# Kernel optimization log

Measured on AMD Instinct MI355X. Metric: run time of the kernel, lower is better.

Reference implementation:

```python
import jax, jax.numpy as jnp
import numpy as np

B, NQ, NK, C = 16, 8, 4096, 256
H = W = 64
HEADS = 8
CI = 128          # embedding_dim // attention_downsample_rate
HD = CI // HEADS  # per-head dim
EPS = float(np.finfo(np.float32).tiny)


def _gumbel_topk(scores, noise, n):
    # iterative gumbel-softmax top-k relaxation with straight-through hard k-hot
    g = scores + noise
    khot = jnp.zeros_like(g)
    onehot = jnp.zeros_like(g)
    for _ in range(n):
        g = g + jnp.log(jnp.maximum(1.0 - onehot, EPS))
        onehot = jax.nn.softmax(g, axis=-1)
        khot = khot + onehot
    _, ind = jax.lax.top_k(khot, n)
    rows = jnp.arange(khot.shape[0])[:, None]
    hard = jnp.zeros_like(khot).at[rows, ind].set(1.0)
    ret = hard - jax.lax.stop_gradient(khot) + khot  # == hard numerically
    return ret, jnp.sort(ind, axis=1)  # sorted idx = row-major order of boolean-mask select


def _sample_points(pe, content, ret, idx):
    # pe [H,W,C], content [b,H,W,C], ret [b,HW] k-hot, idx [b,k] sorted
    b = ret.shape[0]
    m = ret.reshape(b, H, W, 1)
    pe_m = (pe[None] * m).reshape(b, H * W, -1)
    c_m = (content * m).reshape(b, H * W, -1)
    take = lambda a: jnp.take_along_axis(a, idx[:, :, None], axis=1)
    return take(pe_m), take(c_m)


def _mlp(x, W1, b1, W2, b2, W3, b3):
    x = jax.nn.relu(x @ W1 + b1)
    x = jax.nn.relu(x @ W2 + b2)
    return x @ W3 + b3


def _forward(queries, keys, query_pe, key_pe, guiding_embedding, gumbel_p, gumbel_n,
             static_uncertain, static_refined, Wq, bq, Wk, bk, Wv, bv, Wo, bo,
             uW1, ub1, uW2, ub2, uW3, ub3, rW1, rb1, rW2, rb2, rW3, rb3,
             pe_gauss, point_pos, point_neg, n_sample_points):
    b = queries.shape[0]
    g = guiding_embedding.reshape(b, C, H * W).transpose(0, 2, 1)  # [b, HW, C]
    g = g * keys  # elementwise gating -> new guiding embedding

    # cross attention token -> image (internal dim CI, HEADS heads)
    def split_heads(x, Wx, bx):
        return (x @ Wx + bx).reshape(b, -1, HEADS, HD).transpose(0, 2, 1, 3)
    qh = split_heads(queries + query_pe, Wq, bq)
    kh = split_heads(g + key_pe, Wk, bk)
    vh = split_heads(g, Wv, bv)
    attn = jax.nn.softmax(jnp.einsum('bhqd,bhkd->bhqk', qh, kh) / np.float32(np.sqrt(HD)), axis=-1)
    out = jnp.einsum('bhqk,bhkd->bhqd', attn, vh).transpose(0, 2, 1, 3).reshape(b, -1, CI)
    queries = out @ Wo + bo  # [b, NQ, C]

    q1 = queries[:, 1, :]
    unc_tok = _mlp(jnp.concatenate([jnp.broadcast_to(static_uncertain, (b, C)), q1], -1),
                   uW1, ub1, uW2, ub2, uW3, ub3)
    ref_tok = _mlp(jnp.concatenate([jnp.broadcast_to(static_refined, (b, C)), q1], -1),
                   rW1, rb1, rW2, rb2, rW3, rb3)

    img = g.transpose(0, 2, 1)  # [b, C, HW]
    unc_norm = jax.nn.sigmoid(jnp.einsum('bc,bcn->bn', unc_tok, img))
    ref_mask = jnp.einsum('bc,bcn->bn', ref_tok, img)
    coarse_mask = jnp.einsum('bc,bcn->bn', q1, img)

    queries = jnp.concatenate([queries[:, 0:1], ref_tok[:, None, :], queries[:, 2:]], axis=1)

    # point-sampling reference map + gumbel-softmax top-k (training-path math)
    ref_map = unc_norm * (jax.nn.sigmoid(ref_mask) - jax.nn.sigmoid(coarse_mask))  # [b, HW]
    ret_p, idx_p = _gumbel_topk(ref_map, gumbel_p, n_sample_points)
    ret_n, idx_n = _gumbel_topk(-ref_map, gumbel_n, n_sample_points)

    # random fourier positional encoding of the 64x64 grid (SAM PositionEmbeddingRandom)
    xs = (jnp.arange(W, dtype=jnp.float32) + 0.5) / W
    ys = (jnp.arange(H, dtype=jnp.float32) + 0.5) / H
    coords = jnp.stack([jnp.tile(xs[None, :], (H, 1)), jnp.tile(ys[:, None], (1, W))], axis=-1)
    proj = ((2.0 * coords - 1.0) @ pe_gauss) * np.float32(2.0 * np.pi)  # [H, W, C//2]
    pe = jnp.concatenate([jnp.sin(proj), jnp.cos(proj)], axis=-1)       # [H, W, C]

    # F.interpolate of a 64x64 map to (64,64) is the identity here
    content = (keys + g).reshape(b, H, W, C)

    sp_pe, sp_c = _sample_points(pe, content, ret_p, idx_p)
    sn_pe, sn_c = _sample_points(pe, content, ret_n, idx_n)
    sp_pe = sp_pe + point_pos  # prompt_encoder.point_embeddings[1]
    sn_pe = sn_pe + point_neg  # prompt_encoder.point_embeddings[0]

    query_pe = jnp.concatenate([query_pe, sp_pe, sn_pe], axis=1)
    queries = jnp.concatenate([queries, sp_c, sn_c], axis=1)
    # pack (queries, query_pe) into one array for a single-output reference
    return jnp.concatenate([queries, query_pe], axis=1)  # [b, 2*(NQ+2k), C]


def setup_inputs():
    key = jax.random.key(0)
    ks = iter(jax.random.split(key, 48))
    n = lambda shape, s=1.0: jax.random.normal(next(ks), shape, jnp.float32) * s
    z = lambda shape: jnp.zeros(shape, jnp.float32)
    return {
        'queries': n((B, NQ, C)),
        'keys': n((B, NK, C)),
        'query_pe': n((B, NQ, C)),
        'key_pe': n((B, NK, C)),
        'guiding_embedding': n((B, C, H, W)),
        'gumbel_p': jax.random.gumbel(next(ks), (B, NK), jnp.float32),
        'gumbel_n': jax.random.gumbel(next(ks), (B, NK), jnp.float32),
        'static_uncertain': n((C,), 0.02),
        'static_refined': n((C,), 0.02),
        'Wq': n((C, CI), 0.02), 'bq': z((CI,)),
        'Wk': n((C, CI), 0.02), 'bk': z((CI,)),
        'Wv': n((C, CI), 0.02), 'bv': z((CI,)),
        'Wo': n((CI, C), 0.02), 'bo': z((C,)),
        'uW1': n((2 * C, C // 4), 0.05), 'ub1': z((C // 4,)),
        'uW2': n((C // 4, C // 4), 0.05), 'ub2': z((C // 4,)),
        'uW3': n((C // 4, C), 0.05), 'ub3': z((C,)),
        'rW1': n((2 * C, C // 4), 0.05), 'rb1': z((C // 4,)),
        'rW2': n((C // 4, C // 4), 0.05), 'rb2': z((C // 4,)),
        'rW3': n((C // 4, C), 0.05), 'rb3': z((C,)),
        'pe_gauss': n((2, C // 2)),
        'point_pos': n((C,), 0.02),
        'point_neg': n((C,), 0.02),
        'n_sample_points': 4,
    }


def reference(queries, keys, query_pe, key_pe, guiding_embedding, gumbel_p, gumbel_n,
              static_uncertain, static_refined, Wq, bq, Wk, bk, Wv, bv, Wo, bo,
              uW1, ub1, uW2, ub2, uW3, ub3, rW1, rb1, rW2, rb2, rW3, rb3,
              pe_gauss, point_pos, point_neg, n_sample_points):
    return _forward(queries, keys, query_pe, key_pe, guiding_embedding, gumbel_p, gumbel_n,
                    static_uncertain, static_refined, Wq, bq, Wk, bk, Wv, bv, Wo, bo,
                    uW1, ub1, uW2, ub2, uW3, ub3, rW1, rb1, rW2, rb2, rW3, rb3,
                    pe_gauss, point_pos, point_neg, n_sample_points)
```

## Files before the change

kernel.cpp:

```cpp
#include <hip/hip_runtime.h>

#define BB 16
#define NQn 8
#define NK 4096
#define CC 256
#define NHEADS 8
#define CIn 128
#define HDn 16
#define NHQ 64
#define EPS_TINY 1.17549435e-38f

constexpr size_t OFF_QK   = 0;
constexpr size_t OFF_QBK  = OFF_QK  + (size_t)BB*CC*NHQ;
constexpr size_t OFF_SC   = OFF_QBK + (size_t)BB*NHQ;
constexpr size_t OFF_MP   = OFF_SC  + (size_t)BB*NK*NHQ;
constexpr size_t OFF_SP   = OFF_MP  + (size_t)BB*32*NHQ;
constexpr size_t OFF_M    = OFF_SP  + (size_t)BB*32*NHQ;
constexpr size_t OFF_RS   = OFF_M   + (size_t)BB*NHQ;
constexpr size_t OFF_AVP  = OFF_RS  + (size_t)BB*NHQ;
constexpr size_t OFF_QATT = OFF_AVP + (size_t)BB*16*NHQ*CC;
constexpr size_t OFF_UNC  = OFF_QATT+ (size_t)BB*NQn*CC;
constexpr size_t OFF_REFT = OFF_UNC + (size_t)BB*CC;
constexpr size_t OFF_RMAP = OFF_REFT+ (size_t)BB*CC;
constexpr size_t OFF_IDX  = OFF_RMAP+ (size_t)BB*NK;
constexpr size_t OFF_RV   = OFF_IDX + 128;
constexpr size_t OFF_G    = OFF_RV  + 128;

__global__ __launch_bounds__(256) void k1_qside(
    const float* __restrict__ queries, const float* __restrict__ query_pe,
    const float* __restrict__ Wq, const float* __restrict__ bq,
    const float* __restrict__ Wk, const float* __restrict__ bk,
    float* __restrict__ ws)
{
  int b = blockIdx.x >> 3, q = blockIdx.x & 7, t = threadIdx.x;
  __shared__ float x[CC];
  __shared__ float qh[CIn];
  x[t] = queries[(b*NQn+q)*CC + t] + query_pe[(b*NQn+q)*CC + t];
  __syncthreads();
  if (t < CIn) {
    float a = bq[t];
    for (int c = 0; c < CC; ++c) a += x[c]*Wq[c*CIn + t];
    qh[t] = a * 0.25f;
  }
  __syncthreads();
  float* Qk = ws + OFF_QK;
  #pragma unroll
  for (int h = 0; h < NHEADS; ++h) {
    float a = 0.f;
    #pragma unroll
    for (int d = 0; d < HDn; ++d) a += qh[h*HDn+d] * Wk[t*CIn + h*HDn + d];
    Qk[((size_t)b*CC + t)*NHQ + h*NQn + q] = a;
  }
  if (t < NHEADS) {
    float a = 0.f;
    #pragma unroll
    for (int d = 0; d < HDn; ++d) a += qh[t*HDn+d] * bk[t*HDn+d];
    (ws + OFF_QBK)[b*NHQ + t*NQn + q] = a;
  }
}

__global__ __launch_bounds__(256) void k2_scores(
    const float* __restrict__ keys, const float* __restrict__ key_pe,
    const float* __restrict__ guiding, float* __restrict__ ws)
{
  int b = blockIdx.y, n0 = blockIdx.x * 64, t = threadIdx.x;
  __shared__ __align__(16) float Xs[64][36];
  __shared__ __align__(16) float Qs[32][64];
  __shared__ float Gt[32][65];
  const float* Qk = ws + OFF_QK + (size_t)b*CC*NHQ;
  float* G = ws + OFF_G;
  int tx = t & 15, ty = t >> 4;
  int xr  = t >> 3;
  int xc4 = (t & 7) * 4;
  int lane = t & 63, wv = t >> 6;
  float acc[4][4] = {};

  for (int c0 = 0; c0 < CC; c0 += 32) {
    size_t base0 = ((size_t)b*NK + n0 + xr)*CC + c0 + xc4;
    size_t base1 = base0 + (size_t)32*CC;
    float4 kp0 = *(const float4*)&keys[base0];
    float4 kp1 = *(const float4*)&keys[base1];
    float4 pp0 = *(const float4*)&key_pe[base0];
    float4 pp1 = *(const float4*)&key_pe[base1];
    float qp[8];
    #pragma unroll
    for (int i = 0; i < 8; ++i) {
      int l = i*256 + t;
      qp[i] = Qk[(size_t)(c0 + (l>>6))*NHQ + (l & 63)];
    }
    #pragma unroll
    for (int i = 0; i < 8; ++i)
      Gt[wv*8 + i][lane] = guiding[((size_t)b*CC + c0 + wv*8 + i)*NK + n0 + lane];
    __syncthreads();
    #pragma unroll
    for (int i = 0; i < 8; ++i) {
      int l = i*256 + t;
      Qs[l>>6][l&63] = qp[i];
    }
    {
      float4 g0, g1;
      g0.x = kp0.x * Gt[xc4+0][xr];    g0.y = kp0.y * Gt[xc4+1][xr];
      g0.z = kp0.z * Gt[xc4+2][xr];    g0.w = kp0.w * Gt[xc4+3][xr];
      g1.x = kp1.x * Gt[xc4+0][xr+32]; g1.y = kp1.y * Gt[xc4+1][xr+32];
      g1.z = kp1.z * Gt[xc4+2][xr+32]; g1.w = kp1.w * Gt[xc4+3][xr+32];
      *(float4*)&G[base0] = g0;
      *(float4*)&G[base1] = g1;
      float4 x0, x1;
      x0.x = g0.x+pp0.x; x0.y = g0.y+pp0.y; x0.z = g0.z+pp0.z; x0.w = g0.w+pp0.w;
      x1.x = g1.x+pp1.x; x1.y = g1.y+pp1.y; x1.z = g1.z+pp1.z; x1.w = g1.w+pp1.w;
      *(float4*)&Xs[xr][xc4]    = x0;
      *(float4*)&Xs[xr+32][xc4] = x1;
    }
    __syncthreads();
    #pragma unroll
    for (int cb = 0; cb < 8; ++cb) {
      float4 xf[4];
      #pragma unroll
      for (int i = 0; i < 4; ++i) xf[i] = *(const float4*)&Xs[4*ty+i][4*cb];
      #pragma unroll
      for (int u = 0; u < 4; ++u) {
        float4 qf = *(const float4*)&Qs[4*cb+u][4*tx];
        float xu[4] = { ((const float*)&xf[0])[u], ((const float*)&xf[1])[u],
                        ((const float*)&xf[2])[u], ((const float*)&xf[3])[u] };
        float qu[4] = { qf.x, qf.y, qf.z, qf.w };
        #pragma unroll
        for (int i = 0; i < 4; ++i)
          #pragma unroll
          for (int j = 0; j < 4; ++j) acc[i][j] += xu[i]*qu[j];
      }
    }
  }
  const float* qbk = ws + OFF_QBK + (size_t)b*NHQ;
  float qb[4] = {qbk[4*tx], qbk[4*tx+1], qbk[4*tx+2], qbk[4*tx+3]};
  float* sc = ws + OFF_SC + ((size_t)b*NK + n0)*NHQ;
  #pragma unroll
  for (int i = 0; i < 4; ++i) {
    float4 o;
    o.x = acc[i][0]+qb[0]; o.y = acc[i][1]+qb[1]; o.z = acc[i][2]+qb[2]; o.w = acc[i][3]+qb[3];
    *(float4*)&sc[(4*ty + i)*NHQ + 4*tx] = o;
  }
}

__global__ __launch_bounds__(256) void k3a_stats(float* __restrict__ ws)
{
  int b = blockIdx.y, sb = blockIdx.x, t = threadIdx.x;
  int hq = t & 63, r = t >> 6;
  const float* sc = ws + OFF_SC + ((size_t)b*NK + sb*128)*NHQ;
  float m = -INFINITY, s = 0.f;
  for (int i = 0; i < 32; ++i) {
    float v = sc[(r + 4*i)*NHQ + hq];
    if (v > m) { s = s*expf(m - v) + 1.f; m = v; } else { s += expf(v - m); }
  }
  __shared__ float rm[256], rs[256];
  rm[t] = m; rs[t] = s;
  __syncthreads();
  if (t < 64) {
    float m0=rm[t], m1=rm[t+64], m2=rm[t+128], m3=rm[t+192];
    float mm = fmaxf(fmaxf(m0,m1), fmaxf(m2,m3));
    float ss = rs[t]*expf(m0-mm) + rs[t+64]*expf(m1-mm) + rs[t+128]*expf(m2-mm) + rs[t+192]*expf(m3-mm);
    (ws + OFF_MP)[(b*32 + sb)*NHQ + t] = mm;
    (ws + OFF_SP)[(b*32 + sb)*NHQ + t] = ss;
  }
}

__global__ __launch_bounds__(64) void k3b_combine(float* __restrict__ ws)
{
  int b = blockIdx.x, hq = threadIdx.x;
  const float* mp = ws + OFF_MP + (size_t)b*32*NHQ;
  const float* sp = ws + OFF_SP + (size_t)b*32*NHQ;
  float m = -INFINITY;
  #pragma unroll
  for (int i = 0; i < 32; ++i) m = fmaxf(m, mp[i*NHQ+hq]);
  float s = 0.f;
  #pragma unroll
  for (int i = 0; i < 32; ++i) s += sp[i*NHQ+hq]*expf(mp[i*NHQ+hq]-m);
  (ws+OFF_M)[b*NHQ+hq] = m;
  (ws+OFF_RS)[b*NHQ+hq] = 1.0f/s;
}

__global__ __launch_bounds__(256) void k4_av(float* __restrict__ ws)
{
  int kb = blockIdx.x, ch = blockIdx.y, b = blockIdx.z, t = threadIdx.x;
  int k0 = kb * 256, cbase = ch * 64;
  __shared__ __align__(16) float gld[32][68];
  __shared__ __align__(16) float wld[32][64];
  __shared__ float mv[64], rv[64];
  if (t < 64) { mv[t] = (ws+OFF_M)[b*NHQ+t]; rv[t] = (ws+OFF_RS)[b*NHQ+t]; }
  int hq0 = (t & 15) * 4, c0 = (t >> 4) * 4;
  int sr = t >> 4, sc4 = (t & 15) * 4;
  float accf[4][4] = {};
  const float* sc = ws + OFF_SC;
  const float* G  = ws + OFF_G;
  __syncthreads();
  for (int kk = 0; kk < 256; kk += 32) {
    #pragma unroll
    for (int p = 0; p < 2; ++p)
      *(float4*)&gld[p*16 + sr][sc4] =
        *(const float4*)&G[((size_t)b*NK + k0+kk + p*16 + sr)*CC + cbase + sc4];
    #pragma unroll
    for (int i = 0; i < 8; ++i) {
      int l = i*256 + t; int k = l >> 6, hq = l & 63;
      float v = sc[((size_t)b*NK + k0+kk+k)*NHQ + hq];
      wld[k][hq] = expf(v - mv[hq]) * rv[hq];
    }
    __syncthreads();
    #pragma unroll 4
    for (int k = 0; k < 32; ++k) {
      float4 w4 = *(const float4*)&wld[k][hq0];
      float4 gv = *(const float4*)&gld[k][c0];
      float wq[4] = {w4.x, w4.y, w4.z, w4.w};
      float gq[4] = {gv.x, gv.y, gv.z, gv.w};
      #pragma unroll
      for (int i = 0; i < 4; ++i)
        #pragma unroll
        for (int j = 0; j < 4; ++j) accf[i][j] += wq[i]*gq[j];
    }
    __syncthreads();
  }
  float* avp = ws + OFF_AVP + (((size_t)b*16 + kb)*NHQ)*CC;
  #pragma unroll
  for (int i = 0; i < 4; ++i) {
    float4 o;
    o.x = accf[i][0]; o.y = accf[i][1]; o.z = accf[i][2]; o.w = accf[i][3];
    *(float4*)&avp[(size_t)(hq0 + i)*CC + cbase + c0] = o;
  }
}

__global__ __launch_bounds__(256) void k56_attout(
    const float* __restrict__ Wv, const float* __restrict__ bv,
    const float* __restrict__ Wo, const float* __restrict__ bo,
    float* __restrict__ ws)
{
  int b = blockIdx.x >> 3, q = blockIdx.x & 7, t = threadIdx.x;
  __shared__ float avs[NHEADS][CC];
  __shared__ float outv[CIn];
  const float* avp = ws + OFF_AVP;
  #pragma unroll
  for (int h = 0; h < NHEADS; ++h) {
    int hq = h*NQn + q;
    float a = 0.f;
    #pragma unroll 4
    for (int kb = 0; kb < 16; ++kb)
      a += avp[(((size_t)b*16 + kb)*NHQ + hq)*CC + t];
    avs[h][t] = a;
  }
  __syncthreads();
  if (t < CIn) {
    int h = t >> 4;
    float a = bv[t];
    for (int c = 0; c < CC; ++c) a += avs[h][c]*Wv[c*CIn + t];
    outv[t] = a;
  }
  __syncthreads();
  float a = bo[t];
  for (int ci = 0; ci < CIn; ++ci) a += outv[ci]*Wo[ci*CC + t];
  (ws+OFF_QATT)[((size_t)b*NQn + q)*CC + t] = a;
}

__global__ __launch_bounds__(256) void k7_mlps(
    const float* __restrict__ su, const float* __restrict__ sr,
    const float* __restrict__ uW1, const float* __restrict__ ub1,
    const float* __restrict__ uW2, const float* __restrict__ ub2,
    const float* __restrict__ uW3, const float* __restrict__ ub3,
    const float* __restrict__ rW1, const float* __restrict__ rb1,
    const float* __restrict__ rW2, const float* __restrict__ rb2,
    const float* __restrict__ rW3, const float* __restrict__ rb3,
    float* __restrict__ ws)
{
  int b = blockIdx.x, t = threadIdx.x;
  __shared__ float xs[768];
  __shared__ float h1[2][64], h2[2][64];
  xs[t] = su[t];
  xs[256+t] = (ws+OFF_QATT)[((size_t)b*NQn + 1)*CC + t];
  xs[512+t] = sr[t];
  __syncthreads();
  if (t < 128) {
    int which = t >> 6, o = t & 63;
    const float* W1 = which ? rW1 : uW1;
    const float* b1 = which ? rb1 : ub1;
    int base = which ? 512 : 0;
    float a = b1[o];
    for (int i = 0; i < 256; ++i) a += xs[base+i]*W1[i*64 + o];
    for (int i = 0; i < 256; ++i) a += xs[256+i]*W1[(256+i)*64 + o];
    h1[which][o] = fmaxf(a, 0.f);
  }
  __syncthreads();
  if (t < 128) {
    int which = t >> 6, o = t & 63;
    const float* W2 = which ? rW2 : uW2;
    const float* b2 = which ? rb2 : ub2;
    float a = b2[o];
    #pragma unroll 8
    for (int i = 0; i < 64; ++i) a += h1[which][i]*W2[i*64+o];
    h2[which][o] = fmaxf(a, 0.f);
  }
  __syncthreads();
  {
    float a = ub3[t];
    #pragma unroll 8
    for (int i = 0; i < 64; ++i) a += h2[0][i]*uW3[i*CC + t];
    (ws+OFF_UNC)[b*CC + t] = a;
    float a2 = rb3[t];
    #pragma unroll 8
    for (int i = 0; i < 64; ++i) a2 += h2[1][i]*rW3[i*CC + t];
    (ws+OFF_REFT)[b*CC + t] = a2;
  }
}

__global__ __launch_bounds__(256) void k8_masks(float* __restrict__ ws)
{
  int b = blockIdx.y, t = threadIdx.x;
  int wave = t >> 6, lane = t & 63;
  __shared__ float q1s[CC], us[CC], rts[CC];
  q1s[t] = (ws+OFF_QATT)[((size_t)b*NQn+1)*CC + t];
  us[t]  = (ws+OFF_UNC)[b*CC + t];
  rts[t] = (ws+OFF_REFT)[b*CC + t];
  __syncthreads();
  float q1v[4], usv[4], rtv[4];
  #pragma unroll
  for (int u = 0; u < 4; ++u) {
    q1v[u] = q1s[lane*4+u]; usv[u] = us[lane*4+u]; rtv[u] = rts[lane*4+u];
  }
  const float* G = ws + OFF_G;
  float* rmap = ws + OFF_RMAP + (size_t)b*NK;
  int n_base = blockIdx.x*64 + wave*16;
  for (int r = 0; r < 16; ++r) {
    int n = n_base + r;
    float4 gv = *(const float4*)&G[((size_t)b*NK + n)*CC + lane*4];
    float aq = gv.x*q1v[0] + gv.y*q1v[1] + gv.z*q1v[2] + gv.w*q1v[3];
    float au = gv.x*usv[0] + gv.y*usv[1] + gv.z*usv[2] + gv.w*usv[3];
    float ar = gv.x*rtv[0] + gv.y*rtv[1] + gv.z*rtv[2] + gv.w*rtv[3];
    #pragma unroll
    for (int s = 1; s < 64; s <<= 1) {
      aq += __shfl_xor(aq, s, 64);
      au += __shfl_xor(au, s, 64);
      ar += __shfl_xor(ar, s, 64);
    }
    if (lane == 0) {
      float un = 1.f/(1.f+expf(-au));
      rmap[n] = un * (1.f/(1.f+expf(-ar)) - 1.f/(1.f+expf(-aq)));
    }
  }
}

__global__ __launch_bounds__(256) void k9_gumbel(
    const float* __restrict__ gp, const float* __restrict__ gn,
    float* __restrict__ ws)
{
  int sign = blockIdx.x, b = blockIdx.y, t = threadIdx.x;
  int wave = t >> 6, lane = t & 63;
  const float* noise = sign ? gn : gp;
  const float* rmap = ws + OFF_RMAP + (size_t)b*NK;
  float g[16], kh[16], oh[16];
  #pragma unroll
  for (int i = 0; i < 16; ++i) {
    int n = i*256 + t;
    float scv = rmap[n];
    if (sign) scv = -scv;
    g[i] = scv + noise[(size_t)b*NK + n];
    kh[i] = 0.f; oh[i] = 0.f;
  }
  __shared__ float wred[8];
  __shared__ float selV[16];
  __shared__ int   selIdx[16];
  for (int it = 0; it < 4; ++it) {
    if (it > 0) {
      #pragma unroll
      for (int i = 0; i < 16; ++i) g[i] += logf(fmaxf(1.f - oh[i], EPS_TINY));
    }
    float m = g[0];
    #pragma unroll
    for (int i = 1; i < 16; ++i) m = fmaxf(m, g[i]);
    #pragma unroll
    for (int s = 1; s < 64; s <<= 1) m = fmaxf(m, __shfl_xor(m, s, 64));
    if (lane == 0) wred[wave] = m;
    __syncthreads();
    m = fmaxf(fmaxf(wred[0], wred[1]), fmaxf(wred[2], wred[3]));
    float e[16], ls = 0.f;
    #pragma unroll
    for (int i = 0; i < 16; ++i) { e[i] = expf(g[i]-m); ls += e[i]; }
    #pragma unroll
    for (int s = 1; s < 64; s <<= 1) ls += __shfl_xor(ls, s, 64);
    if (lane == 0) wred[4+wave] = ls;
    __syncthreads();
    float ssum = wred[4]+wred[5]+wred[6]+wred[7];
    #pragma unroll
    for (int i = 0; i < 16; ++i) { oh[i] = e[i]/ssum; kh[i] += oh[i]; }
  }
  int id[4]; float rr[4];
  for (int j = 0; j < 4; ++j) {
    float bv = kh[0]; int bi = t;
    #pragma unroll
    for (int i = 1; i < 16; ++i) {
      if (kh[i] > bv) { bv = kh[i]; bi = i*256 + t; }
    }
    #pragma unroll
    for (int s = 1; s < 64; s <<= 1) {
      float ov = __shfl_xor(bv, s, 64);
      int   oi = __shfl_xor(bi, s, 64);
      if (ov > bv || (ov == bv && oi < bi)) { bv = ov; bi = oi; }
    }
    if (lane == 0) { selV[j*4+wave] = bv; selIdx[j*4+wave] = bi; }
    __syncthreads();
    bv = selV[j*4]; bi = selIdx[j*4];
    #pragma unroll
    for (int w = 1; w < 4; ++w) {
      float ov = selV[j*4+w]; int oi = selIdx[j*4+w];
      if (ov > bv || (ov == bv && oi < bi)) { bv = ov; bi = oi; }
    }
    id[j] = bi; rr[j] = (1.f - bv) + bv;
    if ((bi & 255) == t) kh[bi >> 8] = -1.f;
  }
  if (t == 0) {
    for (int a = 0; a < 3; ++a)
      for (int c2 = a+1; c2 < 4; ++c2)
        if (id[c2] < id[a]) { int ti=id[a]; id[a]=id[c2]; id[c2]=ti; float tr=rr[a]; rr[a]=rr[c2]; rr[c2]=tr; }
    int* iout = (int*)(ws + OFF_IDX);
    float* rout = ws + OFF_RV;
    for (int j = 0; j < 4; ++j) {
      iout[(sign*BB + b)*4 + j] = id[j];
      rout[(sign*BB + b)*4 + j] = rr[j];
    }
  }
}

__global__ __launch_bounds__(256) void k10_out(
    const float* __restrict__ keys, const float* __restrict__ query_pe,
    const float* __restrict__ point_pos, const float* __restrict__ point_neg,
    const float* __restrict__ pe_gauss,
    float* __restrict__ ws, float* __restrict__ out)
{
  int b = blockIdx.y, r = blockIdx.x, t = threadIdx.x;
  const float* G = ws + OFF_G;
  float val;
  if (r < 8) {
    val = (r == 1) ? (ws+OFF_REFT)[b*CC + t]
                   : (ws+OFF_QATT)[((size_t)b*NQn + r)*CC + t];
  } else if (r < 16) {
    int j = r - 8; int sign = j >> 2; int jj = j & 3;
    int idx = ((const int*)(ws+OFF_IDX))[(sign*BB + b)*4 + jj];
    float rvv = (ws+OFF_RV)[(sign*BB + b)*4 + jj];
    float kv = keys[((size_t)b*NK + idx)*CC + t];
    float gv = G[((size_t)b*NK + idx)*CC + t];
    val = (kv + gv) * rvv;
  } else if (r < 24) {
    val = query_pe[((size_t)b*NQn + (r-16))*CC + t];
  } else {
    int j = r - 24; int sign = j >> 2; int jj = j & 3;
    int idx = ((const int*)(ws+OFF_IDX))[(sign*BB + b)*4 + jj];
    float rvv = (ws+OFF_RV)[(sign*BB + b)*4 + jj];
    const float* point = sign ? point_neg : point_pos;
    int h = idx >> 6, w = idx & 63;
    float x = (w + 0.5f)/64.f, y = (h + 0.5f)/64.f;
    int jf = (t < 128) ? t : (t - 128);
    float proj = ((2.f*x - 1.f)*pe_gauss[jf] + (2.f*y - 1.f)*pe_gauss[128 + jf]) * 6.28318530717958647692f;
    float sv = (t < 128) ? sinf(proj) : cosf(proj);
    val = sv*rvv + point[t];
  }
  out[((size_t)b*32 + r)*CC + t] = val;
}

extern "C" void kernel_launch(void* const* d_in, const int* in_sizes, int n_in,
                              void* d_out, int out_size, void* d_ws, size_t ws_size,
                              hipStream_t stream)
{
  const float* queries   = (const float*)d_in[0];
  const float* keys      = (const float*)d_in[1];
  const float* query_pe  = (const float*)d_in[2];
  const float* key_pe    = (const float*)d_in[3];
  const float* guiding   = (const float*)d_in[4];
  const float* gumbel_p  = (const float*)d_in[5];
  const float* gumbel_n  = (const float*)d_in[6];
  const float* s_unc     = (const float*)d_in[7];
  const float* s_ref     = (const float*)d_in[8];
  const float* Wq  = (const float*)d_in[9];   const float* bq  = (const float*)d_in[10];
  const float* Wk  = (const float*)d_in[11];  const float* bk  = (const float*)d_in[12];
  const float* Wv  = (const float*)d_in[13];  const float* bv  = (const float*)d_in[14];
  const float* Wo  = (const float*)d_in[15];  const float* bo  = (const float*)d_in[16];
  const float* uW1 = (const float*)d_in[17];  const float* ub1 = (const float*)d_in[18];
  const float* uW2 = (const float*)d_in[19];  const float* ub2 = (const float*)d_in[20];
  const float* uW3 = (const float*)d_in[21];  const float* ub3 = (const float*)d_in[22];
  const float* rW1 = (const float*)d_in[23];  const float* rb1 = (const float*)d_in[24];
  const float* rW2 = (const float*)d_in[25];  const float* rb2 = (const float*)d_in[26];
  const float* rW3 = (const float*)d_in[27];  const float* rb3 = (const float*)d_in[28];
  const float* pe_gauss  = (const float*)d_in[29];
  const float* point_pos = (const float*)d_in[30];
  const float* point_neg = (const float*)d_in[31];
  float* ws = (float*)d_ws;
  float* out = (float*)d_out;

  k1_qside  <<<dim3(BB*NQn),    256, 0, stream>>>(queries, query_pe, Wq, bq, Wk, bk, ws);
  k2_scores <<<dim3(64, BB),    256, 0, stream>>>(keys, key_pe, guiding, ws);
  k3a_stats <<<dim3(32, BB),    256, 0, stream>>>(ws);
  k3b_combine<<<dim3(BB),        64, 0, stream>>>(ws);
  k4_av     <<<dim3(16, 4, BB), 256, 0, stream>>>(ws);
  k56_attout<<<dim3(BB*NQn),    256, 0, stream>>>(Wv, bv, Wo, bo, ws);
  k7_mlps   <<<dim3(BB),        256, 0, stream>>>(s_unc, s_ref, uW1, ub1, uW2, ub2, uW3, ub3,
                                                  rW1, rb1, rW2, rb2, rW3, rb3, ws);
  k8_masks  <<<dim3(64, BB),    256, 0, stream>>>(ws);
  k9_gumbel <<<dim3(2, BB),     256, 0, stream>>>(gumbel_p, gumbel_n, ws);
  k10_out   <<<dim3(32, BB),    256, 0, stream>>>(keys, query_pe, point_pos, point_neg,
                                                  pe_gauss, ws, out);
}
```

Baseline: 221.1 us.

## Prefetch next chunk in score kernel, precompute softmax weights, simplify AV kernel

The score kernel now gives each thread one key row and 16 head-query columns, and it loads the next 32-channel chunk of keys, key_pe, guiding and Qk into registers while the current chunk is being computed. Shared padding is also adjusted. A new kernel applies exp and normalisation to the score buffer in place, so the AV kernel no longer recomputes expf per tile. The AV kernel drops shared-memory tiling and streams weights and G straight from global memory, with each thread accumulating 16 outputs. This adds one extra read and write pass over the score buffer and one extra launch, and the AV loads now depend on the cache to get reuse.

```diff
diff --git a/kernel.cpp b/kernel.cpp
--- a/kernel.cpp
+++ b/kernel.cpp
@@ -64,80 +64,89 @@
     const float* __restrict__ guiding, float* __restrict__ ws)
 {
   int b = blockIdx.y, n0 = blockIdx.x * 64, t = threadIdx.x;
-  __shared__ __align__(16) float Xs[64][36];
+  __shared__ __align__(16) float Xs[64][34];
   __shared__ __align__(16) float Qs[32][64];
-  __shared__ float Gt[32][65];
+  __shared__ float Gt[32][66];
   const float* Qk = ws + OFF_QK + (size_t)b*CC*NHQ;
   float* G = ws + OFF_G;
-  int tx = t & 15, ty = t >> 4;
-  int xr  = t >> 3;
-  int xc4 = (t & 7) * 4;
-  int lane = t & 63, wv = t >> 6;
-  float acc[4][4] = {};
-
-  for (int c0 = 0; c0 < CC; c0 += 32) {
-    size_t base0 = ((size_t)b*NK + n0 + xr)*CC + c0 + xc4;
-    size_t base1 = base0 + (size_t)32*CC;
-    float4 kp0 = *(const float4*)&keys[base0];
-    float4 kp1 = *(const float4*)&keys[base1];
-    float4 pp0 = *(const float4*)&key_pe[base0];
-    float4 pp1 = *(const float4*)&key_pe[base1];
-    float qp[8];
-    #pragma unroll
-    for (int i = 0; i < 8; ++i) {
-      int l = i*256 + t;
-      qp[i] = Qk[(size_t)(c0 + (l>>6))*NHQ + (l & 63)];
-    }
+  const int lane = t & 63, wv = t >> 6;
+  const int hqb = wv * 16;
+  const int xr = t >> 2, xco = (t & 3) * 8;
+  const int qc = t >> 3, qh = (t & 7) * 8;
+  float acc[16] = {};
+
+  float gld[8];
+  float4 k0v, k1v, p0v, p1v, q0v, q1v;
+  {
     #pragma unroll
     for (int i = 0; i < 8; ++i)
-      Gt[wv*8 + i][lane] = guiding[((size_t)b*CC + c0 + wv*8 + i)*NK + n0 + lane];
+      gld[i] = guiding[((size_t)b*CC + wv*8 + i)*NK + n0 + lane];
+    size_t kb = ((size_t)b*NK + n0 + xr)*CC + xco;
+    k0v = *(const float4*)&keys[kb];     k1v = *(const float4*)&keys[kb+4];
+    p0v = *(const float4*)&key_pe[kb];   p1v = *(const float4*)&key_pe[kb+4];
+    q0v = *(const float4*)&Qk[(size_t)qc*NHQ + qh];
+    q1v = *(const float4*)&Qk[(size_t)qc*NHQ + qh + 4];
+  }
+
+  for (int ch = 0; ch < 8; ++ch) {
+    int c0 = ch * 32;
+    #pragma unroll
+    for (int i = 0; i < 8; ++i) Gt[wv*8 + i][lane] = gld[i];
     __syncthreads();
-    #pragma unroll
-    for (int i = 0; i < 8; ++i) {
-      int l = i*256 + t;
-      Qs[l>>6][l&63] = qp[i];
-    }
     {
-      float4 g0, g1;
-      g0.x = kp0.x * Gt[xc4+0][xr];    g0.y = kp0.y * Gt[xc4+1][xr];
-      g0.z = kp0.z * Gt[xc4+2][xr];    g0.w = kp0.w * Gt[xc4+3][xr];
-      g1.x = kp1.x * Gt[xc4+0][xr+32]; g1.y = kp1.y * Gt[xc4+1][xr+32];
-      g1.z = kp1.z * Gt[xc4+2][xr+32]; g1.w = kp1.w * Gt[xc4+3][xr+32];
-      *(float4*)&G[base0] = g0;
-      *(float4*)&G[base1] = g1;
-      float4 x0, x1;
-      x0.x = g0.x+pp0.x; x0.y = g0.y+pp0.y; x0.z = g0.z+pp0.z; x0.w = g0.w+pp0.w;
-      x1.x = g1.x+pp1.x; x1.y = g1.y+pp1.y; x1.z = g1.z+pp1.z; x1.w = g1.w+pp1.w;
-      *(float4*)&Xs[xr][xc4]    = x0;
-      *(float4*)&Xs[xr+32][xc4] = x1;
+      size_t kb = ((size_t)b*NK + n0 + xr)*CC + c0 + xco;
+      float g0x = k0v.x * Gt[xco+0][xr], g0y = k0v.y * Gt[xco+1][xr];
+      float g0z = k0v.z * Gt[xco+2][xr], g0w = k0v.w * Gt[xco+3][xr];
+      float g1x = k1v.x * Gt[xco+4][xr], g1y = k1v.y * Gt[xco+5][xr];
+      float g1z = k1v.z * Gt[xco+6][xr], g1w = k1v.w * Gt[xco+7][xr];
+      float4 gs0; gs0.x=g0x; gs0.y=g0y; gs0.z=g0z; gs0.w=g0w;
+      float4 gs1; gs1.x=g1x; gs1.y=g1y; gs1.z=g1z; gs1.w=g1w;
+      *(float4*)&G[kb]   = gs0;
+      *(float4*)&G[kb+4] = gs1;
+      float x0 = g0x+p0v.x, x1 = g0y+p0v.y, x2 = g0z+p0v.z, x3 = g0w+p0v.w;
+      float x4 = g1x+p1v.x, x5 = g1y+p1v.y, x6 = g1z+p1v.z, x7 = g1w+p1v.w;
+      *(float2*)&Xs[xr][xco+0] = make_float2(x0, x1);
+      *(float2*)&Xs[xr][xco+2] = make_float2(x2, x3);
+      *(float2*)&Xs[xr][xco+4] = make_float2(x4, x5);
+      *(float2*)&Xs[xr][xco+6] = make_float2(x6, x7);
+      *(float4*)&Qs[qc][qh]   = q0v;
+      *(float4*)&Qs[qc][qh+4] = q1v;
     }
     __syncthreads();
-    #pragma unroll
-    for (int cb = 0; cb < 8; ++cb) {
-      float4 xf[4];
+    if (ch < 7) {
+      int c1 = c0 + 32;
       #pragma unroll
-      for (int i = 0; i < 4; ++i) xf[i] = *(const float4*)&Xs[4*ty+i][4*cb];
-      #pragma unroll
-      for (int u = 0; u < 4; ++u) {
-        float4 qf = *(const float4*)&Qs[4*cb+u][4*tx];
-        float xu[4] = { ((const float*)&xf[0])[u], ((const float*)&xf[1])[u],
-                        ((const float*)&xf[2])[u], ((const float*)&xf[3])[u] };
-        float qu[4] = { qf.x, qf.y, qf.z, qf.w };
-        #pragma unroll
-        for (int i = 0; i < 4; ++i)
-          #pragma unroll
-          for (int j = 0; j < 4; ++j) acc[i][j] += xu[i]*qu[j];
-      }
-    }
-  }
-  const float* qbk = ws + OFF_QBK + (size_t)b*NHQ;
-  float qb[4] = {qbk[4*tx], qbk[4*tx+1], qbk[4*tx+2], qbk[4*tx+3]};
-  float* sc = ws + OFF_SC + ((size_t)b*NK + n0)*NHQ;
-  #pragma unroll
-  for (int i = 0; i < 4; ++i) {
+      for (int i = 0; i < 8; ++i)
+        gld[i] = guiding[((size_t)b*CC + c1 + wv*8 + i)*NK + n0 + lane];
+      size_t kb = ((size_t)b*NK + n0 + xr)*CC + c1 + xco;
+      k0v = *(const float4*)&keys[kb];     k1v = *(const float4*)&keys[kb+4];
+      p0v = *(const float4*)&key_pe[kb];   p1v = *(const float4*)&key_pe[kb+4];
+      q0v = *(const float4*)&Qk[(size_t)(c1 + qc)*NHQ + qh];
+      q1v = *(const float4*)&Qk[(size_t)(c1 + qc)*NHQ + qh + 4];
+    }
+    #pragma unroll 8
+    for (int c = 0; c < 32; ++c) {
+      float xv = Xs[lane][c];
+      float4 qa = *(const float4*)&Qs[c][hqb];
+      float4 qb4 = *(const float4*)&Qs[c][hqb+4];
+      float4 qc4 = *(const float4*)&Qs[c][hqb+8];
+      float4 qd = *(const float4*)&Qs[c][hqb+12];
+      acc[0]  += xv*qa.x;  acc[1]  += xv*qa.y;  acc[2]  += xv*qa.z;  acc[3]  += xv*qa.w;
+      acc[4]  += xv*qb4.x; acc[5]  += xv*qb4.y; acc[6]  += xv*qb4.z; acc[7]  += xv*qb4.w;
+      acc[8]  += xv*qc4.x; acc[9]  += xv*qc4.y; acc[10] += xv*qc4.z; acc[11] += xv*qc4.w;
+      acc[12] += xv*qd.x;  acc[13] += xv*qd.y;  acc[14] += xv*qd.z;  acc[15] += xv*qd.w;
+    }
+  }
+  const float* qbk = ws + OFF_QBK + (size_t)b*NHQ + hqb;
+  float* sc = ws + OFF_SC + ((size_t)b*NK + n0 + lane)*NHQ + hqb;
+  #pragma unroll
+  for (int i4 = 0; i4 < 4; ++i4) {
     float4 o;
-    o.x = acc[i][0]+qb[0]; o.y = acc[i][1]+qb[1]; o.z = acc[i][2]+qb[2]; o.w = acc[i][3]+qb[3];
-    *(float4*)&sc[(4*ty + i)*NHQ + 4*tx] = o;
+    o.x = acc[i4*4+0] + qbk[i4*4+0];
+    o.y = acc[i4*4+1] + qbk[i4*4+1];
+    o.z = acc[i4*4+2] + qbk[i4*4+2];
+    o.w = acc[i4*4+3] + qbk[i4*4+3];
+    *(float4*)&sc[i4*4] = o;
   }
 }
 
@@ -178,52 +187,57 @@
   (ws+OFF_RS)[b*NHQ+hq] = 1.0f/s;
 }
 
+__global__ __launch_bounds__(256) void k3c_weights(float* __restrict__ ws)
+{
+  int b = blockIdx.y, t = threadIdx.x;
+  size_t f = (size_t)blockIdx.x * 2048 + (size_t)t * 8;
+  float* sc = ws + OFF_SC + (size_t)b*NK*NHQ + f;
+  const float* m  = ws + OFF_M  + (size_t)b*NHQ;
+  const float* rs = ws + OFF_RS + (size_t)b*NHQ;
+  int hq0 = (int)(f & 63);
+  float4 v0 = *(const float4*)&sc[0];
+  float4 v1 = *(const float4*)&sc[4];
+  float o[8] = {v0.x,v0.y,v0.z,v0.w, v1.x,v1.y,v1.z,v1.w};
+  #pragma unroll
+  for (int j = 0; j < 8; ++j) o[j] = expf(o[j] - m[hq0+j]) * rs[hq0+j];
+  float4 w0; w0.x=o[0]; w0.y=o[1]; w0.z=o[2]; w0.w=o[3];
+  float4 w1; w1.x=o[4]; w1.y=o[5]; w1.z=o[6]; w1.w=o[7];
+  *(float4*)&sc[0] = w0;
+  *(float4*)&sc[4] = w1;
+}
+
 __global__ __launch_bounds__(256) void k4_av(float* __restrict__ ws)
 {
-  int kb = blockIdx.x, ch = blockIdx.y, b = blockIdx.z, t = threadIdx.x;
-  int k0 = kb * 256, cbase = ch * 64;
-  __shared__ __align__(16) float gld[32][68];
-  __shared__ __align__(16) float wld[32][64];
-  __shared__ float mv[64], rv[64];
-  if (t < 64) { mv[t] = (ws+OFF_M)[b*NHQ+t]; rv[t] = (ws+OFF_RS)[b*NHQ+t]; }
-  int hq0 = (t & 15) * 4, c0 = (t >> 4) * 4;
-  int sr = t >> 4, sc4 = (t & 15) * 4;
-  float accf[4][4] = {};
-  const float* sc = ws + OFF_SC;
-  const float* G  = ws + OFF_G;
-  __syncthreads();
-  for (int kk = 0; kk < 256; kk += 32) {
-    #pragma unroll
-    for (int p = 0; p < 2; ++p)
-      *(float4*)&gld[p*16 + sr][sc4] =
-        *(const float4*)&G[((size_t)b*NK + k0+kk + p*16 + sr)*CC + cbase + sc4];
-    #pragma unroll
-    for (int i = 0; i < 8; ++i) {
-      int l = i*256 + t; int k = l >> 6, hq = l & 63;
-      float v = sc[((size_t)b*NK + k0+kk+k)*NHQ + hq];
-      wld[k][hq] = expf(v - mv[hq]) * rv[hq];
-    }
-    __syncthreads();
-    #pragma unroll 4
-    for (int k = 0; k < 32; ++k) {
-      float4 w4 = *(const float4*)&wld[k][hq0];
-      float4 gv = *(const float4*)&gld[k][c0];
-      float wq[4] = {w4.x, w4.y, w4.z, w4.w};
-      float gq[4] = {gv.x, gv.y, gv.z, gv.w};
-      #pragma unroll
-      for (int i = 0; i < 4; ++i)
-        #pragma unroll
-        for (int j = 0; j < 4; ++j) accf[i][j] += wq[i]*gq[j];
-    }
-    __syncthreads();
-  }
-  float* avp = ws + OFF_AVP + (((size_t)b*16 + kb)*NHQ)*CC;
-  #pragma unroll
-  for (int i = 0; i < 4; ++i) {
-    float4 o;
-    o.x = accf[i][0]; o.y = accf[i][1]; o.z = accf[i][2]; o.w = accf[i][3];
-    *(float4*)&avp[(size_t)(hq0 + i)*CC + cbase + c0] = o;
-  }
+  int kb = blockIdx.x, cq = blockIdx.y, b = blockIdx.z, t = threadIdx.x;
+  int lane = t & 63, wv = t >> 6;
+  int c = cq*64 + lane, hqb = wv*16;
+  size_t kbase = (size_t)b*NK + (size_t)kb*256;
+  const float* Wp = ws + OFF_SC + kbase*NHQ + hqb;
+  const float* Gp = ws + OFF_G  + kbase*CC + c;
+  float acc[16] = {};
+  for (int k = 0; k < 256; k += 2) {
+    float g0 = Gp[(size_t)k*CC];
+    float g1 = Gp[(size_t)(k+1)*CC];
+    float4 a0 = *(const float4*)&Wp[(size_t)k*NHQ];
+    float4 a1 = *(const float4*)&Wp[(size_t)k*NHQ + 4];
+    float4 a2 = *(const float4*)&Wp[(size_t)k*NHQ + 8];
+    float4 a3 = *(const float4*)&Wp[(size_t)k*NHQ + 12];
+    float4 b0 = *(const float4*)&Wp[(size_t)(k+1)*NHQ];
+    float4 b1 = *(const float4*)&Wp[(size_t)(k+1)*NHQ + 4];
+    float4 b2 = *(const float4*)&Wp[(size_t)(k+1)*NHQ + 8];
+    float4 b3 = *(const float4*)&Wp[(size_t)(k+1)*NHQ + 12];
+    acc[0]+=a0.x*g0;  acc[1]+=a0.y*g0;  acc[2]+=a0.z*g0;  acc[3]+=a0.w*g0;
+    acc[4]+=a1.x*g0;  acc[5]+=a1.y*g0;  acc[6]+=a1.z*g0;  acc[7]+=a1.w*g0;
+    acc[8]+=a2.x*g0;  acc[9]+=a2.y*g0;  acc[10]+=a2.z*g0; acc[11]+=a2.w*g0;
+    acc[12]+=a3.x*g0; acc[13]+=a3.y*g0; acc[14]+=a3.z*g0; acc[15]+=a3.w*g0;
+    acc[0]+=b0.x*g1;  acc[1]+=b0.y*g1;  acc[2]+=b0.z*g1;  acc[3]+=b0.w*g1;
+    acc[4]+=b1.x*g1;  acc[5]+=b1.y*g1;  acc[6]+=b1.z*g1;  acc[7]+=b1.w*g1;
+    acc[8]+=b2.x*g1;  acc[9]+=b2.y*g1;  acc[10]+=b2.z*g1; acc[11]+=b2.w*g1;
+    acc[12]+=b3.x*g1; acc[13]+=b3.y*g1; acc[14]+=b3.z*g1; acc[15]+=b3.w*g1;
+  }
+  float* avp = ws + OFF_AVP + (((size_t)b*16 + kb)*NHQ + hqb)*CC + c;
+  #pragma unroll
+  for (int i = 0; i < 16; ++i) avp[(size_t)i*CC] = acc[i];
 }
 
 __global__ __launch_bounds__(256) void k56_attout(
@@ -493,6 +507,7 @@
   k2_scores <<<dim3(64, BB),    256, 0, stream>>>(keys, key_pe, guiding, ws);
   k3a_stats <<<dim3(32, BB),    256, 0, stream>>>(ws);
   k3b_combine<<<dim3(BB),        64, 0, stream>>>(ws);
+  k3c_weights<<<dim3(128, BB),  256, 0, stream>>>(ws);
   k4_av     <<<dim3(16, 4, BB), 256, 0, stream>>>(ws);
   k56_attout<<<dim3(BB*NQn),    256, 0, stream>>>(Wv, bv, Wo, bo, ws);
   k7_mlps   <<<dim3(BB),        256, 0, stream>>>(s_unc, s_ref, uW1, ub1, uW2, ub2, uW3, ub3,
```

Result: slower. 330.7 us (+49.6%).

## Shrink score/AV tiles, prefetch next chunk, precompute softmax weights in separate kernel

Applied to the files above, without the earlier changes.

k2_scores now handles 32 keys per block instead of 64, doubling the grid. It software-prefetches the next channel chunk of guiding, keys, key_pe and Qk into registers while the current chunk is being computed. The softmax exp/normalize moves out of k4_av into a new elementwise k3c_weights kernel that rewrites the scores in place, and k4_av splits heads across two blocks with smaller per-thread tiles. k8_masks also doubles its grid with fewer rows per block. The aim is more blocks for occupancy and latency hiding, and no repeated exp work across the four channel-quarter blocks, at the cost of an extra launch, an extra pass over the scores, and lower per-thread reuse.

```diff
diff --git a/kernel.cpp b/kernel.cpp
--- a/kernel.cpp
+++ b/kernel.cpp
@@ -59,38 +59,39 @@
   }
 }
 
-__global__ __launch_bounds__(256) void k2_scores(
+__global__ __launch_bounds__(256, 8) void k2_scores(
     const float* __restrict__ keys, const float* __restrict__ key_pe,
     const float* __restrict__ guiding, float* __restrict__ ws)
 {
-  int b = blockIdx.y, n0 = blockIdx.x * 64, t = threadIdx.x;
-  __shared__ __align__(16) float Xs[64][36];
+  int b = blockIdx.y, n0 = blockIdx.x * 32, t = threadIdx.x;
+  __shared__ __align__(16) float Xs[32][36];
   __shared__ __align__(16) float Qs[32][64];
-  __shared__ float Gt[32][65];
+  __shared__ float Gt[32][33];
   const float* Qk = ws + OFF_QK + (size_t)b*CC*NHQ;
   float* G = ws + OFF_G;
-  int tx = t & 15, ty = t >> 4;
-  int xr  = t >> 3;
-  int xc4 = (t & 7) * 4;
-  int lane = t & 63, wv = t >> 6;
-  float acc[4][4] = {};
-
-  for (int c0 = 0; c0 < CC; c0 += 32) {
-    size_t base0 = ((size_t)b*NK + n0 + xr)*CC + c0 + xc4;
-    size_t base1 = base0 + (size_t)32*CC;
-    float4 kp0 = *(const float4*)&keys[base0];
-    float4 kp1 = *(const float4*)&keys[base1];
-    float4 pp0 = *(const float4*)&key_pe[base0];
-    float4 pp1 = *(const float4*)&key_pe[base1];
-    float qp[8];
+  const int tx = t & 15, ty = t >> 4;
+  const int xr = t >> 3, xc4 = (t & 7) * 4;
+  const int gn = t & 31, gc0 = (t >> 5) * 4;
+  float acc[2][4] = {};
+
+  float gld[4]; float4 kp, pp; float qp[8];
+  {
+    #pragma unroll
+    for (int i = 0; i < 4; ++i)
+      gld[i] = guiding[((size_t)b*CC + gc0 + i)*NK + n0 + gn];
+    size_t kb = ((size_t)b*NK + n0 + xr)*CC + xc4;
+    kp = *(const float4*)&keys[kb];
+    pp = *(const float4*)&key_pe[kb];
     #pragma unroll
     for (int i = 0; i < 8; ++i) {
       int l = i*256 + t;
-      qp[i] = Qk[(size_t)(c0 + (l>>6))*NHQ + (l & 63)];
-    }
-    #pragma unroll
-    for (int i = 0; i < 8; ++i)
-      Gt[wv*8 + i][lane] = guiding[((size_t)b*CC + c0 + wv*8 + i)*NK + n0 + lane];
+      qp[i] = Qk[(size_t)(l>>6)*NHQ + (l & 63)];
+    }
+  }
+  for (int ch = 0; ch < 8; ++ch) {
+    int c0 = ch*32;
+    #pragma unroll
+    for (int i = 0; i < 4; ++i) Gt[gc0 + i][gn] = gld[i];
     __syncthreads();
     #pragma unroll
     for (int i = 0; i < 8; ++i) {
@@ -98,35 +99,42 @@
       Qs[l>>6][l&63] = qp[i];
     }
     {
-      float4 g0, g1;
-      g0.x = kp0.x * Gt[xc4+0][xr];    g0.y = kp0.y * Gt[xc4+1][xr];
-      g0.z = kp0.z * Gt[xc4+2][xr];    g0.w = kp0.w * Gt[xc4+3][xr];
-      g1.x = kp1.x * Gt[xc4+0][xr+32]; g1.y = kp1.y * Gt[xc4+1][xr+32];
-      g1.z = kp1.z * Gt[xc4+2][xr+32]; g1.w = kp1.w * Gt[xc4+3][xr+32];
-      *(float4*)&G[base0] = g0;
-      *(float4*)&G[base1] = g1;
-      float4 x0, x1;
-      x0.x = g0.x+pp0.x; x0.y = g0.y+pp0.y; x0.z = g0.z+pp0.z; x0.w = g0.w+pp0.w;
-      x1.x = g1.x+pp1.x; x1.y = g1.y+pp1.y; x1.z = g1.z+pp1.z; x1.w = g1.w+pp1.w;
-      *(float4*)&Xs[xr][xc4]    = x0;
-      *(float4*)&Xs[xr+32][xc4] = x1;
-    }
-    __syncthreads();
+      size_t kbase = ((size_t)b*NK + n0 + xr)*CC + c0 + xc4;
+      float4 g4;
+      g4.x = kp.x * Gt[xc4+0][xr];
+      g4.y = kp.y * Gt[xc4+1][xr];
+      g4.z = kp.z * Gt[xc4+2][xr];
+      g4.w = kp.w * Gt[xc4+3][xr];
+      *(float4*)&G[kbase] = g4;
+      float4 o; o.x=g4.x+pp.x; o.y=g4.y+pp.y; o.z=g4.z+pp.z; o.w=g4.w+pp.w;
+      *(float4*)&Xs[xr][xc4] = o;
+    }
+    __syncthreads();
+    if (ch < 7) {
+      int c1 = c0 + 32;
+      #pragma unroll
+      for (int i = 0; i < 4; ++i)
+        gld[i] = guiding[((size_t)b*CC + c1 + gc0 + i)*NK + n0 + gn];
+      size_t kb2 = ((size_t)b*NK + n0 + xr)*CC + c1 + xc4;
+      kp = *(const float4*)&keys[kb2];
+      pp = *(const float4*)&key_pe[kb2];
+      #pragma unroll
+      for (int i = 0; i < 8; ++i) {
+        int l = i*256 + t;
+        qp[i] = Qk[(size_t)(c1 + (l>>6))*NHQ + (l & 63)];
+      }
+    }
     #pragma unroll
     for (int cb = 0; cb < 8; ++cb) {
-      float4 xf[4];
-      #pragma unroll
-      for (int i = 0; i < 4; ++i) xf[i] = *(const float4*)&Xs[4*ty+i][4*cb];
+      float4 x0 = *(const float4*)&Xs[2*ty][4*cb];
+      float4 x1 = *(const float4*)&Xs[2*ty+1][4*cb];
       #pragma unroll
       for (int u = 0; u < 4; ++u) {
         float4 qf = *(const float4*)&Qs[4*cb+u][4*tx];
-        float xu[4] = { ((const float*)&xf[0])[u], ((const float*)&xf[1])[u],
-                        ((const float*)&xf[2])[u], ((const float*)&xf[3])[u] };
-        float qu[4] = { qf.x, qf.y, qf.z, qf.w };
-        #pragma unroll
-        for (int i = 0; i < 4; ++i)
-          #pragma unroll
-          for (int j = 0; j < 4; ++j) acc[i][j] += xu[i]*qu[j];
+        float xu0 = ((const float*)&x0)[u];
+        float xu1 = ((const float*)&x1)[u];
+        acc[0][0] += xu0*qf.x; acc[0][1] += xu0*qf.y; acc[0][2] += xu0*qf.z; acc[0][3] += xu0*qf.w;
+        acc[1][0] += xu1*qf.x; acc[1][1] += xu1*qf.y; acc[1][2] += xu1*qf.z; acc[1][3] += xu1*qf.w;
       }
     }
   }
@@ -134,10 +142,10 @@
   float qb[4] = {qbk[4*tx], qbk[4*tx+1], qbk[4*tx+2], qbk[4*tx+3]};
   float* sc = ws + OFF_SC + ((size_t)b*NK + n0)*NHQ;
   #pragma unroll
-  for (int i = 0; i < 4; ++i) {
+  for (int i = 0; i < 2; ++i) {
     float4 o;
     o.x = acc[i][0]+qb[0]; o.y = acc[i][1]+qb[1]; o.z = acc[i][2]+qb[2]; o.w = acc[i][3]+qb[3];
-    *(float4*)&sc[(4*ty + i)*NHQ + 4*tx] = o;
+    *(float4*)&sc[(size_t)(2*ty + i)*NHQ + 4*tx] = o;
   }
 }
 
@@ -178,52 +186,63 @@
   (ws+OFF_RS)[b*NHQ+hq] = 1.0f/s;
 }
 
-__global__ __launch_bounds__(256) void k4_av(float* __restrict__ ws)
-{
-  int kb = blockIdx.x, ch = blockIdx.y, b = blockIdx.z, t = threadIdx.x;
-  int k0 = kb * 256, cbase = ch * 64;
+__global__ __launch_bounds__(256) void k3c_weights(float* __restrict__ ws)
+{
+  int b = blockIdx.y, t = threadIdx.x;
+  size_t f = (size_t)blockIdx.x * 2048 + (size_t)t * 8;
+  float* sc = ws + OFF_SC + (size_t)b*NK*NHQ + f;
+  const float* m  = ws + OFF_M  + (size_t)b*NHQ;
+  const float* rs = ws + OFF_RS + (size_t)b*NHQ;
+  int hq0 = (int)(f & 63);
+  float4 v0 = *(const float4*)&sc[0];
+  float4 v1 = *(const float4*)&sc[4];
+  float o[8] = {v0.x,v0.y,v0.z,v0.w, v1.x,v1.y,v1.z,v1.w};
+  #pragma unroll
+  for (int j = 0; j < 8; ++j) o[j] = expf(o[j] - m[hq0+j]) * rs[hq0+j];
+  float4 w0; w0.x=o[0]; w0.y=o[1]; w0.z=o[2]; w0.w=o[3];
+  float4 w1; w1.x=o[4]; w1.y=o[5]; w1.z=o[6]; w1.w=o[7];
+  *(float4*)&sc[0] = w0;
+  *(float4*)&sc[4] = w1;
+}
+
+__global__ __launch_bounds__(256, 8) void k4_av(float* __restrict__ ws)
+{
+  int xb = blockIdx.x, cq = blockIdx.y, b = blockIdx.z, t = threadIdx.x;
+  int kb = xb >> 1, hh = (xb & 1) * 32;
+  int k0 = kb * 256, cbase = cq * 64;
   __shared__ __align__(16) float gld[32][68];
-  __shared__ __align__(16) float wld[32][64];
-  __shared__ float mv[64], rv[64];
-  if (t < 64) { mv[t] = (ws+OFF_M)[b*NHQ+t]; rv[t] = (ws+OFF_RS)[b*NHQ+t]; }
-  int hq0 = (t & 15) * 4, c0 = (t >> 4) * 4;
-  int sr = t >> 4, sc4 = (t & 15) * 4;
-  float accf[4][4] = {};
-  const float* sc = ws + OFF_SC;
+  __shared__ __align__(16) float wld[32][36];
+  const int hq0 = (t & 7) * 4, c0 = (t >> 3) * 2;
+  const int sr = t >> 4, sc4 = (t & 15) * 4;
+  float acc[4][2] = {};
+  const float* Wp = ws + OFF_SC;
   const float* G  = ws + OFF_G;
-  __syncthreads();
   for (int kk = 0; kk < 256; kk += 32) {
+    __syncthreads();
     #pragma unroll
     for (int p = 0; p < 2; ++p)
       *(float4*)&gld[p*16 + sr][sc4] =
         *(const float4*)&G[((size_t)b*NK + k0+kk + p*16 + sr)*CC + cbase + sc4];
     #pragma unroll
-    for (int i = 0; i < 8; ++i) {
-      int l = i*256 + t; int k = l >> 6, hq = l & 63;
-      float v = sc[((size_t)b*NK + k0+kk+k)*NHQ + hq];
-      wld[k][hq] = expf(v - mv[hq]) * rv[hq];
+    for (int i = 0; i < 4; ++i) {
+      int l = i*256 + t; int k = l >> 5, hqw = l & 31;
+      wld[k][hqw] = Wp[((size_t)b*NK + k0+kk+k)*NHQ + hh + hqw];
     }
     __syncthreads();
     #pragma unroll 4
     for (int k = 0; k < 32; ++k) {
       float4 w4 = *(const float4*)&wld[k][hq0];
-      float4 gv = *(const float4*)&gld[k][c0];
-      float wq[4] = {w4.x, w4.y, w4.z, w4.w};
-      float gq[4] = {gv.x, gv.y, gv.z, gv.w};
-      #pragma unroll
-      for (int i = 0; i < 4; ++i)
-        #pragma unroll
-        for (int j = 0; j < 4; ++j) accf[i][j] += wq[i]*gq[j];
-    }
-    __syncthreads();
-  }
-  float* avp = ws + OFF_AVP + (((size_t)b*16 + kb)*NHQ)*CC;
-  #pragma unroll
-  for (int i = 0; i < 4; ++i) {
-    float4 o;
-    o.x = accf[i][0]; o.y = accf[i][1]; o.z = accf[i][2]; o.w = accf[i][3];
-    *(float4*)&avp[(size_t)(hq0 + i)*CC + cbase + c0] = o;
-  }
+      float2 g2 = *(const float2*)&gld[k][c0];
+      acc[0][0] += w4.x*g2.x; acc[0][1] += w4.x*g2.y;
+      acc[1][0] += w4.y*g2.x; acc[1][1] += w4.y*g2.y;
+      acc[2][0] += w4.z*g2.x; acc[2][1] += w4.z*g2.y;
+      acc[3][0] += w4.w*g2.x; acc[3][1] += w4.w*g2.y;
+    }
+  }
+  float* avp = ws + OFF_AVP + (((size_t)b*16 + kb)*NHQ + hh + hq0)*CC + cbase + c0;
+  #pragma unroll
+  for (int i = 0; i < 4; ++i)
+    *(float2*)&avp[(size_t)i*CC] = make_float2(acc[i][0], acc[i][1]);
 }
 
 __global__ __launch_bounds__(256) void k56_attout(
@@ -323,8 +342,8 @@
   }
   const float* G = ws + OFF_G;
   float* rmap = ws + OFF_RMAP + (size_t)b*NK;
-  int n_base = blockIdx.x*64 + wave*16;
-  for (int r = 0; r < 16; ++r) {
+  int n_base = blockIdx.x*32 + wave*8;
+  for (int r = 0; r < 8; ++r) {
     int n = n_base + r;
     float4 gv = *(const float4*)&G[((size_t)b*NK + n)*CC + lane*4];
     float aq = gv.x*q1v[0] + gv.y*q1v[1] + gv.z*q1v[2] + gv.w*q1v[3];
@@ -490,14 +509,15 @@
   float* out = (float*)d_out;
 
   k1_qside  <<<dim3(BB*NQn),    256, 0, stream>>>(queries, query_pe, Wq, bq, Wk, bk, ws);
-  k2_scores <<<dim3(64, BB),    256, 0, stream>>>(keys, key_pe, guiding, ws);
+  k2_scores <<<dim3(128, BB),   256, 0, stream>>>(keys, key_pe, guiding, ws);
   k3a_stats <<<dim3(32, BB),    256, 0, stream>>>(ws);
   k3b_combine<<<dim3(BB),        64, 0, stream>>>(ws);
-  k4_av     <<<dim3(16, 4, BB), 256, 0, stream>>>(ws);
+  k3c_weights<<<dim3(128, BB),  256, 0, stream>>>(ws);
+  k4_av     <<<dim3(32, 4, BB), 256, 0, stream>>>(ws);
   k56_attout<<<dim3(BB*NQn),    256, 0, stream>>>(Wv, bv, Wo, bo, ws);
   k7_mlps   <<<dim3(BB),        256, 0, stream>>>(s_unc, s_ref, uW1, ub1, uW2, ub2, uW3, ub3,
                                                   rW1, rb1, rW2, rb2, rW3, rb3, ws);
-  k8_masks  <<<dim3(64, BB),    256, 0, stream>>>(ws);
+  k8_masks  <<<dim3(128, BB),   256, 0, stream>>>(ws);
   k9_gumbel <<<dim3(2, BB),     256, 0, stream>>>(gumbel_p, gumbel_n, ws);
   k10_out   <<<dim3(32, BB),    256, 0, stream>>>(keys, query_pe, point_pos, point_neg,
                                                   pe_gauss, ws, out);
```

Result: slower. 250.9 us (+13.5%).
